# Optimization experiments

Measured on AMD Instinct MI355X. Metric: run time of the kernel, lower is better.

Reference implementation:

```python
import jax, jax.numpy as jnp
import numpy as np

D = 1024
H = 16
HD = D // H
EPS = 1e-6


def rms_norm(x, w):
    # x: [..., hd]; compute in float32 like the torch module
    xf = x.astype(jnp.float32)
    rms = jnp.sqrt(jnp.mean(xf * xf, axis=-1, keepdims=True) + EPS)
    return (xf / rms * w.astype(jnp.float32)).astype(x.dtype)


def setup_inputs() -> dict:
    key = jax.random.key(0)
    ks = jax.random.split(key, 6)
    B, S = 2, 2048
    x = jax.random.normal(ks[0], (B, S, D), dtype=jnp.float32)
    Wqkv = jax.random.normal(ks[1], (3 * D, D), dtype=jnp.float32) * (1.0 / np.sqrt(D))
    bqkv = jax.random.normal(ks[2], (3 * D,), dtype=jnp.float32) * 0.02
    Wproj = jax.random.normal(ks[3], (D, D), dtype=jnp.float32) * (1.0 / np.sqrt(D))
    bproj = jax.random.normal(ks[4], (D,), dtype=jnp.float32) * 0.02
    qn_w = jnp.ones((HD,), dtype=jnp.float32)
    kn_w = jnp.ones((HD,), dtype=jnp.float32)
    return {"x": x, "Wqkv": Wqkv, "bqkv": bqkv, "Wproj": Wproj, "bproj": bproj,
            "qn_w": qn_w, "kn_w": kn_w}


def reference(x, Wqkv, bqkv, Wproj, bproj, qn_w, kn_w):
    B, S, _ = x.shape
    # QKV projection: torch Linear is x @ W.T + b
    qkv = x @ Wqkv.T + bqkv                     # [B, S, 3D]
    qkv = qkv.reshape(B, S, 3, H, HD)
    q, k, v = qkv[:, :, 0], qkv[:, :, 1], qkv[:, :, 2]   # each [B, S, H, hd]
    q = rms_norm(q, qn_w)
    k = rms_norm(k, kn_w)
    # move heads forward: [B, H, S, hd]
    q = q.transpose(0, 2, 1, 3)
    k = k.transpose(0, 2, 1, 3)
    v = v.transpose(0, 2, 1, 3)
    scale = 1.0 / np.sqrt(HD)
    scores = jnp.einsum('bhsd,bhtd->bhst', q, k) * scale   # [B, H, S, S] (math backend)
    attn = jax.nn.softmax(scores, axis=-1)
    out = jnp.einsum('bhst,bhtd->bhsd', attn, v)            # [B, H, S, hd]
    out = out.transpose(0, 2, 1, 3).reshape(B, S, D)
    return out @ Wproj.T + bproj
```

## Files before the change

### kernel.cpp

```cpp
#include <hip/hip_runtime.h>
#include <hip/hip_bf16.h>
#include <math.h>

#define D_MODEL 1024
#define NH 16
#define HD 64
#define SEQ 2048
#define BATCH 2
#define NTOK (BATCH*SEQ)

typedef short bf16x8 __attribute__((ext_vector_type(8)));
typedef short s4 __attribute__((ext_vector_type(4)));
typedef float f32x4 __attribute__((ext_vector_type(4)));
typedef unsigned short us4 __attribute__((ext_vector_type(4)));

#define MFMA(a,b,c) __builtin_amdgcn_mfma_f32_16x16x32_bf16(a,b,c,0,0,0)

union bfu { __hip_bfloat16 b; unsigned short u; };
__device__ __forceinline__ unsigned short f2b(float f){ bfu t; t.b = __float2bfloat16(f); return t.u; }
__device__ __forceinline__ float b2f(unsigned short u){ bfu t; t.u = u; return __bfloat162float(t.b); }

__device__ __forceinline__ void g2l16(const unsigned short* g, unsigned short* l){
    __builtin_amdgcn_global_load_lds(
        (const __attribute__((address_space(1))) unsigned int*)g,
        (__attribute__((address_space(3))) unsigned int*)l, 16, 0, 0);
}

#define OFF_X   128L
#define OFF_WQ  (OFF_X  + 4194304L)
#define OFF_BQ  (OFF_WQ + 3145728L)
#define OFF_WP  (OFF_BQ + 3072L)
#define OFF_BP  (OFF_WP + 1048576L)
#define OFF_QN  (OFF_BP + 1024L)
#define OFF_KN  (OFF_QN + 64L)
#define OFF_Q   (OFF_KN + 64L)
#define OFF_K   (OFF_Q  + 4194304L)
#define OFF_V   (OFF_K  + 4194304L)
#define OFF_A   (OFF_V  + 4194304L)

__global__ __launch_bounds__(256) void detect_kernel(
    const unsigned int* __restrict__ xraw, int* __restrict__ flag)
{
    __shared__ int cnt;
    if (threadIdx.x == 0) cnt = 0;
    __syncthreads();
    int local = 0;
    const uint4* x4 = (const uint4*)xraw;
    for (int i = threadIdx.x; i < 8192; i += 256){
        uint4 v = x4[i];
        unsigned int w[4] = {v.x, v.y, v.z, v.w};
        #pragma unroll
        for (int j=0;j<4;j++){
            local += ((w[j] & 0x7F80u) >= 0x4800u);
            local += (((w[j]>>16) & 0x7F80u) >= 0x4800u);
        }
    }
    atomicAdd(&cnt, local);
    __syncthreads();
    if (threadIdx.x == 0) *flag = (cnt > 256) ? 1 : 0;
}

__global__ __launch_bounds__(256) void convert_kernel(
    const void* __restrict__ x,  const void* __restrict__ wq,
    const void* __restrict__ bq, const void* __restrict__ wp,
    const void* __restrict__ bp, const void* __restrict__ qn,
    const void* __restrict__ kn, unsigned short* __restrict__ ws,
    const int* __restrict__ flagp)
{
    const int flag = *flagp;
    long i = (long)blockIdx.x*blockDim.x + threadIdx.x;
    const long stride = (long)gridDim.x*blockDim.x;
    const long NCH = 2098208L;
    for (; i < NCH; i += stride){
        long j = i; const void* src; long off;
        if (j < 1048576L)                  { src = x;  off = OFF_X;  }
        else if ((j -= 1048576L) < 786432L){ src = wq; off = OFF_WQ; }
        else if ((j -= 786432L)  < 768L)   { src = bq; off = OFF_BQ; }
        else if ((j -= 768L)     < 262144L){ src = wp; off = OFF_WP; }
        else if ((j -= 262144L)  < 256L)   { src = bp; off = OFF_BP; }
        else if ((j -= 256L)     < 16L)    { src = qn; off = OFF_QN; }
        else      { j -= 16L;                src = kn; off = OFF_KN; }
        us4 o;
        if (flag){
            float4 v = ((const float4*)src)[j];
            o.x = f2b(v.x); o.y = f2b(v.y); o.z = f2b(v.z); o.w = f2b(v.w);
        } else {
            o = ((const us4*)src)[j];
        }
        *(us4*)(ws + off + j*4) = o;
    }
}

__global__ __launch_bounds__(256) void qkv_kernel(
    const unsigned short* __restrict__ x,
    const unsigned short* __restrict__ Wqkv,
    const unsigned short* __restrict__ bqkv,
    const unsigned short* __restrict__ qn_w,
    const unsigned short* __restrict__ kn_w,
    unsigned short* __restrict__ qbuf,
    unsigned short* __restrict__ kbuf,
    unsigned short* __restrict__ vbuf)
{
    __shared__ __align__(16) unsigned short tA[128*32];
    __shared__ __align__(16) unsigned short tB[128*32];
    const int tid  = threadIdx.x;
    const int w    = tid >> 6, lane = tid & 63, quad = lane >> 4, c = lane & 15;
    const int m0 = blockIdx.y*128, n0 = blockIdx.x*128;
    const int am = (w>>1)*64, bn = (w&1)*64;

    f32x4 acc[4][4];
    for (int mi=0;mi<4;mi++) for (int ni=0;ni<4;ni++) acc[mi][ni] = {0.f,0.f,0.f,0.f};

    const int i0 = tid, i1 = tid + 256;
    const long ga0 = (long)(m0 + (i0>>2))*D_MODEL + (i0&3)*8;
    const long ga1 = (long)(m0 + (i1>>2))*D_MODEL + (i1&3)*8;
    const long gb0 = (long)(n0 + (i0>>2))*D_MODEL + (i0&3)*8;
    const long gb1 = (long)(n0 + (i1>>2))*D_MODEL + (i1&3)*8;

    for (int k0=0;k0<D_MODEL;k0+=32){
        g2l16(x    + ga0 + k0, tA + i0*8);
        g2l16(x    + ga1 + k0, tA + i1*8);
        g2l16(Wqkv + gb0 + k0, tB + i0*8);
        g2l16(Wqkv + gb1 + k0, tB + i1*8);
        __syncthreads();
        bf16x8 a[4], b[4];
        for (int mi=0;mi<4;mi++) a[mi] = *(const bf16x8*)(tA + (am + mi*16 + c)*32 + quad*8);
        for (int ni=0;ni<4;ni++) b[ni] = *(const bf16x8*)(tB + (bn + ni*16 + c)*32 + quad*8);
        for (int mi=0;mi<4;mi++)
            for (int ni=0;ni<4;ni++)
                acc[mi][ni] = MFMA(a[mi], b[ni], acc[mi][ni]);
        __syncthreads();
    }

    const int nw = n0 + bn, mw = m0 + am;
    const int region = nw >> 10;
    const int h      = (nw & 1023) >> 6;
    float bias[4], wn[4];
    for (int ni=0;ni<4;ni++){
        bias[ni] = b2f(bqkv[nw + ni*16 + c]);
        wn[ni]   = 1.0f;
    }
    if (region==0) for (int ni=0;ni<4;ni++) wn[ni] = b2f(qn_w[ni*16+c]);
    if (region==1) for (int ni=0;ni<4;ni++) wn[ni] = b2f(kn_w[ni*16+c]);
    unsigned short* dst = (region==0) ? qbuf : (region==1) ? kbuf : vbuf;

    for (int mi=0;mi<4;mi++){
        for (int ni=0;ni<4;ni++)
            for (int r=0;r<4;r++) acc[mi][ni][r] += bias[ni];

        float scale_r[4];
        if (region < 2){
            for (int r=0;r<4;r++){
                float ss = 0.f;
                for (int ni=0;ni<4;ni++){ float v2 = acc[mi][ni][r]; ss += v2*v2; }
                ss += __shfl_xor(ss, 1, 64);
                ss += __shfl_xor(ss, 2, 64);
                ss += __shfl_xor(ss, 4, 64);
                ss += __shfl_xor(ss, 8, 64);
                scale_r[r] = rsqrtf(ss*(1.0f/64.0f) + 1e-6f);
            }
        } else {
            for (int r=0;r<4;r++) scale_r[r] = 1.0f;
        }

        for (int r=0;r<4;r++){
            int m = mw + mi*16 + quad*4 + r;
            int bidx = m >> 11, s = m & 2047;
            long base = ((long)(bidx*NH + h)*SEQ + s)*HD;
            for (int ni=0;ni<4;ni++)
                dst[base + ni*16 + c] = f2b(acc[mi][ni][r] * scale_r[r] * wn[ni]);
        }
    }
}

__global__ __launch_bounds__(256) void attn_kernel(
    const unsigned short* __restrict__ qbuf,
    const unsigned short* __restrict__ kbuf,
    const unsigned short* __restrict__ vbuf,
    unsigned short* __restrict__ abuf)
{
    const int tid = threadIdx.x, w = tid>>6, lane = tid&63, quad = lane>>4, c = lane&15;
    const int bh = blockIdx.y, qt = blockIdx.x;
    const unsigned short* qb = qbuf + (long)bh*SEQ*HD;
    const unsigned short* kb = kbuf + (long)bh*SEQ*HD;
    const unsigned short* vb = vbuf + (long)bh*SEQ*HD;
    const int qbase = qt*128 + w*32;

    __shared__ __align__(16) short VT[2][80][72];
    __shared__ __align__(16) short P[4][2048];
    short* Pw = &P[w][0];

    for (int i = tid; i < 2*16*72; i += 256){
        int bi = i / 1152, rem = i - bi*1152;
        VT[bi][64 + rem/72][rem%72] = 0;
    }
    __syncthreads();
    if (tid < 128) VT[tid>>6][64][tid&63] = 0x3F80;

    bf16x8 aq[2][2];
    for (int mi=0;mi<2;mi++)
        for (int ks=0;ks<2;ks++)
            aq[mi][ks] = *(const bf16x8*)(qb + (long)(qbase + mi*16 + c)*HD + ks*32 + quad*8);

    f32x4 o[2][5];
    for (int mi=0;mi<2;mi++) for (int nt=0;nt<5;nt++) o[mi][nt] = {0.f,0.f,0.f,0.f};

    const int d0 = (tid & 31)*2;
    const int kg = tid >> 5;

    unsigned int vA[8], vB[8];
    bf16x8 kA[4][2], kB[4][2];

    auto stageV = [&](int key0, unsigned int* vr){
        #pragma unroll
        for (int j=0;j<8;j++)
            vr[j] = *(const unsigned int*)(vb + (long)(key0 + kg*8 + j)*HD + d0);
    };
    auto loadK = [&](int key0, bf16x8 (*kf)[2]){
        #pragma unroll
        for (int mt=0;mt<4;mt++)
            #pragma unroll
            for (int ks=0;ks<2;ks++)
                kf[mt][ks] = *(const bf16x8*)(kb + (long)(key0 + mt*16 + c)*HD + ks*32 + quad*8);
    };
    auto writeV = [&](unsigned int* vr, short (*vt)[72]){
        bf16x8 lo, hi;
        #pragma unroll
        for (int j=0;j<8;j++){
            lo[j] = (short)(vr[j] & 0xffffu);
            hi[j] = (short)(vr[j] >> 16);
        }
        *(bf16x8*)(&vt[d0][kg*8])   = lo;
        *(bf16x8*)(&vt[d0+1][kg*8]) = hi;
    };
    auto compute = [&](short (*vt)[72], bf16x8 (*kf)[2]){
        f32x4 z[4][2];
        #pragma unroll
        for (int mt=0;mt<4;mt++)
            #pragma unroll
            for (int mi=0;mi<2;mi++){
                f32x4 t = {0.f,0.f,0.f,0.f};
                t = MFMA(kf[mt][0], aq[mi][0], t);
                t = MFMA(kf[mt][1], aq[mi][1], t);
                z[mt][mi] = t;
            }
        #pragma unroll
        for (int mt=0;mt<4;mt++){
            const int key8 = mt*2 + (quad>>1);
            #pragma unroll
            for (int mi=0;mi<2;mi++){
                s4 pk;
                #pragma unroll
                for (int r=0;r<4;r++)
                    pk[r] = (short)f2b(exp2f(z[mt][mi][r]*0.18033688f - 17.312340f));
                *(s4*)(Pw + (key8*32 + mi*16 + c)*8 + (quad&1)*4) = pk;
            }
        }
        #pragma unroll
        for (int ks=0;ks<2;ks++){
            bf16x8 bv[5];
            #pragma unroll
            for (int nt=0;nt<5;nt++)
                bv[nt] = *(const bf16x8*)(&vt[nt*16 + c][ks*32 + quad*8]);
            #pragma unroll
            for (int mi=0;mi<2;mi++){
                bf16x8 ap = *(const bf16x8*)(Pw + ((ks*4+quad)*32 + mi*16 + c)*8);
                #pragma unroll
                for (int nt=0;nt<5;nt++)
                    o[mi][nt] = MFMA(ap, bv[nt], o[mi][nt]);
            }
        }
    };

    stageV(0, vA); loadK(0, kA);
    for (int tt=0; tt<16; tt++){
        const int t1 = tt*2 + 1;
        writeV(vA, VT[0]);
        __syncthreads();
        stageV(t1*64, vB); loadK(t1*64, kB);
        compute(VT[0], kA);
        writeV(vB, VT[1]);
        __syncthreads();
        if (tt < 15){ stageV((t1+1)*64, vA); loadK((t1+1)*64, kA); }
        compute(VT[1], kB);
    }

    const int b = bh >> 4, h = bh & 15;
    for (int mi=0;mi<2;mi++)
        for (int r=0;r<4;r++){
            float l = __shfl(o[mi][4][r], (lane & 0x30), 64);
            float inv = 1.0f / l;
            int s = qbase + mi*16 + quad*4 + r;
            long base = ((long)(b*SEQ + s)*NH + h)*HD;
            for (int nt=0;nt<4;nt++)
                abuf[base + nt*16 + c] = f2b(o[mi][nt][r]*inv);
        }
}

__global__ __launch_bounds__(256) void proj_kernel(
    const unsigned short* __restrict__ abuf,
    const unsigned short* __restrict__ Wp,
    const unsigned short* __restrict__ bp,
    void* __restrict__ outv,
    const int* __restrict__ flagp)
{
    __shared__ __align__(16) unsigned short tA[128*32];
    __shared__ __align__(16) unsigned short tB[128*32];
    const int tid  = threadIdx.x;
    const int w    = tid >> 6, lane = tid & 63, quad = lane >> 4, c = lane & 15;
    const int m0 = blockIdx.y*128, n0 = blockIdx.x*128;
    const int am = (w>>1)*64, bn = (w&1)*64;
    const int flag = *flagp;

    f32x4 acc[4][4];
    for (int mi=0;mi<4;mi++) for (int ni=0;ni<4;ni++) acc[mi][ni] = {0.f,0.f,0.f,0.f};

    const int i0 = tid, i1 = tid + 256;
    const long ga0 = (long)(m0 + (i0>>2))*D_MODEL + (i0&3)*8;
    const long ga1 = (long)(m0 + (i1>>2))*D_MODEL + (i1&3)*8;
    const long gb0 = (long)(n0 + (i0>>2))*D_MODEL + (i0&3)*8;
    const long gb1 = (long)(n0 + (i1>>2))*D_MODEL + (i1&3)*8;

    for (int k0=0;k0<D_MODEL;k0+=32){
        g2l16(abuf + ga0 + k0, tA + i0*8);
        g2l16(abuf + ga1 + k0, tA + i1*8);
        g2l16(Wp   + gb0 + k0, tB + i0*8);
        g2l16(Wp   + gb1 + k0, tB + i1*8);
        __syncthreads();
        bf16x8 a[4], b[4];
        for (int mi=0;mi<4;mi++) a[mi] = *(const bf16x8*)(tA + (am + mi*16 + c)*32 + quad*8);
        for (int ni=0;ni<4;ni++) b[ni] = *(const bf16x8*)(tB + (bn + ni*16 + c)*32 + quad*8);
        for (int mi=0;mi<4;mi++)
            for (int ni=0;ni<4;ni++)
                acc[mi][ni] = MFMA(a[mi], b[ni], acc[mi][ni]);
        __syncthreads();
    }

    float bias[4];
    for (int ni=0;ni<4;ni++) bias[ni] = b2f(bp[n0 + bn + ni*16 + c]);

    for (int mi=0;mi<4;mi++)
        for (int r=0;r<4;r++){
            long m = m0 + am + mi*16 + quad*4 + r;
            for (int ni=0;ni<4;ni++){
                float val = acc[mi][ni][r] + bias[ni];
                long idx = m*D_MODEL + n0 + bn + ni*16 + c;
                if (flag) ((float*)outv)[idx] = val;
                else      ((unsigned short*)outv)[idx] = f2b(val);
            }
        }
}

extern "C" void kernel_launch(void* const* d_in, const int* in_sizes, int n_in,
                              void* d_out, int out_size, void* d_ws, size_t ws_size,
                              hipStream_t stream)
{
    unsigned short* ws = (unsigned short*)d_ws;
    int* flag = (int*)d_ws;

    hipLaunchKernelGGL(detect_kernel, dim3(1), dim3(256), 0, stream,
                       (const unsigned int*)d_in[0], flag);
    hipLaunchKernelGGL(convert_kernel, dim3(2048), dim3(256), 0, stream,
                       d_in[0], d_in[1], d_in[2], d_in[3], d_in[4], d_in[5], d_in[6],
                       ws, flag);
    hipLaunchKernelGGL(qkv_kernel,  dim3(24,32), dim3(256), 0, stream,
                       ws+OFF_X, ws+OFF_WQ, ws+OFF_BQ, ws+OFF_QN, ws+OFF_KN,
                       ws+OFF_Q, ws+OFF_K, ws+OFF_V);
    hipLaunchKernelGGL(attn_kernel, dim3(16,32), dim3(256), 0, stream,
                       ws+OFF_Q, ws+OFF_K, ws+OFF_V, ws+OFF_A);
    hipLaunchKernelGGL(proj_kernel, dim3(8,32),  dim3(256), 0, stream,
                       ws+OFF_A, ws+OFF_WP, ws+OFF_BP, d_out, flag);
}
```

Before: 248.0 us.

## Pre-transpose V in a separate kernel and drop LDS staging in attention

After: 407.9 us. +64.5%, slower.

```diff
diff --git a/kernel.cpp b/kernel.cpp
--- a/kernel.cpp
+++ b/kernel.cpp
@@ -19,6 +19,11 @@
 union bfu { __hip_bfloat16 b; unsigned short u; };
 __device__ __forceinline__ unsigned short f2b(float f){ bfu t; t.b = __float2bfloat16(f); return t.u; }
 __device__ __forceinline__ float b2f(unsigned short u){ bfu t; t.u = u; return __bfloat162float(t.b); }
+__device__ __forceinline__ unsigned short f2bf(float f){
+    unsigned int u = __float_as_uint(f);
+    u += 0x7FFFu + ((u >> 16) & 1u);
+    return (unsigned short)(u >> 16);
+}
 
 __device__ __forceinline__ void g2l16(const unsigned short* g, unsigned short* l){
     __builtin_amdgcn_global_load_lds(
@@ -37,6 +42,7 @@
 #define OFF_K   (OFF_Q  + 4194304L)
 #define OFF_V   (OFF_K  + 4194304L)
 #define OFF_A   (OFF_V  + 4194304L)
+#define OFF_VT  (OFF_A  + 4194304L)
 
 __global__ __launch_bounds__(256) void detect_kernel(
     const unsigned int* __restrict__ xraw, int* __restrict__ flag)
@@ -168,54 +174,64 @@
             int bidx = m >> 11, s = m & 2047;
             long base = ((long)(bidx*NH + h)*SEQ + s)*HD;
             for (int ni=0;ni<4;ni++)
-                dst[base + ni*16 + c] = f2b(acc[mi][ni][r] * scale_r[r] * wn[ni]);
-        }
-    }
+                dst[base + ni*16 + c] = f2bf(acc[mi][ni][r] * scale_r[r] * wn[ni]);
+        }
+    }
+}
+
+__global__ __launch_bounds__(256) void vtrans_kernel(
+    const unsigned short* __restrict__ vbuf,
+    unsigned short* __restrict__ vtbuf)
+{
+    const int tid = threadIdx.x;
+    const int bh = blockIdx.y, s0 = blockIdx.x*64;
+    __shared__ __align__(16) unsigned short t[64][72];
+
+    const unsigned short* src = vbuf + (long)bh*SEQ*HD + (long)s0*HD;
+    #pragma unroll
+    for (int it=0; it<2; it++){
+        int idx = tid + it*256;
+        int si = idx >> 3, d0 = (idx & 7)*8;
+        *(bf16x8*)(&t[si][d0]) = *(const bf16x8*)(src + si*HD + d0);
+    }
+    __syncthreads();
+
+    const int d = tid >> 2, sc = (tid & 3)*16;
+    unsigned short* dst = vtbuf + ((long)bh*HD + d)*SEQ + s0 + sc;
+    bf16x8 o0, o1;
+    #pragma unroll
+    for (int j=0;j<8;j++){ o0[j] = t[sc+j][d]; o1[j] = t[sc+8+j][d]; }
+    *(bf16x8*)(dst)     = o0;
+    *(bf16x8*)(dst + 8) = o1;
 }
 
 __global__ __launch_bounds__(256) void attn_kernel(
     const unsigned short* __restrict__ qbuf,
     const unsigned short* __restrict__ kbuf,
-    const unsigned short* __restrict__ vbuf,
+    const unsigned short* __restrict__ vtbuf,
     unsigned short* __restrict__ abuf)
 {
     const int tid = threadIdx.x, w = tid>>6, lane = tid&63, quad = lane>>4, c = lane&15;
     const int bh = blockIdx.y, qt = blockIdx.x;
-    const unsigned short* qb = qbuf + (long)bh*SEQ*HD;
-    const unsigned short* kb = kbuf + (long)bh*SEQ*HD;
-    const unsigned short* vb = vbuf + (long)bh*SEQ*HD;
-    const int qbase = qt*128 + w*32;
-
-    __shared__ __align__(16) short VT[2][80][72];
-    __shared__ __align__(16) short P[4][2048];
+    const unsigned short* qb = qbuf  + (long)bh*SEQ*HD;
+    const unsigned short* kb = kbuf  + (long)bh*SEQ*HD;
+    const unsigned short* vt = vtbuf + (long)bh*HD*SEQ;
+    const int qbase = qt*64 + w*16;
+
+    __shared__ __align__(16) short P[4][1024];
     short* Pw = &P[w][0];
 
-    for (int i = tid; i < 2*16*72; i += 256){
-        int bi = i / 1152, rem = i - bi*1152;
-        VT[bi][64 + rem/72][rem%72] = 0;
-    }
-    __syncthreads();
-    if (tid < 128) VT[tid>>6][64][tid&63] = 0x3F80;
-
-    bf16x8 aq[2][2];
-    for (int mi=0;mi<2;mi++)
-        for (int ks=0;ks<2;ks++)
-            aq[mi][ks] = *(const bf16x8*)(qb + (long)(qbase + mi*16 + c)*HD + ks*32 + quad*8);
-
-    f32x4 o[2][5];
-    for (int mi=0;mi<2;mi++) for (int nt=0;nt<5;nt++) o[mi][nt] = {0.f,0.f,0.f,0.f};
-
-    const int d0 = (tid & 31)*2;
-    const int kg = tid >> 5;
-
-    unsigned int vA[8], vB[8];
+    bf16x8 aq[2];
+    #pragma unroll
+    for (int ks=0;ks<2;ks++)
+        aq[ks] = *(const bf16x8*)(qb + (long)(qbase + c)*HD + ks*32 + quad*8);
+
+    f32x4 o[4];
+    #pragma unroll
+    for (int nt=0;nt<4;nt++) o[nt] = {0.f,0.f,0.f,0.f};
+    float l_loc = 0.f;
+
     bf16x8 kA[4][2], kB[4][2];
-
-    auto stageV = [&](int key0, unsigned int* vr){
-        #pragma unroll
-        for (int j=0;j<8;j++)
-            vr[j] = *(const unsigned int*)(vb + (long)(key0 + kg*8 + j)*HD + d0);
-    };
     auto loadK = [&](int key0, bf16x8 (*kf)[2]){
         #pragma unroll
         for (int mt=0;mt<4;mt++)
@@ -223,78 +239,66 @@
             for (int ks=0;ks<2;ks++)
                 kf[mt][ks] = *(const bf16x8*)(kb + (long)(key0 + mt*16 + c)*HD + ks*32 + quad*8);
     };
-    auto writeV = [&](unsigned int* vr, short (*vt)[72]){
-        bf16x8 lo, hi;
-        #pragma unroll
-        for (int j=0;j<8;j++){
-            lo[j] = (short)(vr[j] & 0xffffu);
-            hi[j] = (short)(vr[j] >> 16);
-        }
-        *(bf16x8*)(&vt[d0][kg*8])   = lo;
-        *(bf16x8*)(&vt[d0+1][kg*8]) = hi;
-    };
-    auto compute = [&](short (*vt)[72], bf16x8 (*kf)[2]){
-        f32x4 z[4][2];
-        #pragma unroll
-        for (int mt=0;mt<4;mt++)
+    loadK(0, kA);
+
+    for (int kt=0; kt<SEQ/64; kt++){
+        const int key0 = kt*64;
+
+        bf16x8 bv[2][4];
+        #pragma unroll
+        for (int ks=0;ks<2;ks++)
             #pragma unroll
-            for (int mi=0;mi<2;mi++){
-                f32x4 t = {0.f,0.f,0.f,0.f};
-                t = MFMA(kf[mt][0], aq[mi][0], t);
-                t = MFMA(kf[mt][1], aq[mi][1], t);
-                z[mt][mi] = t;
-            }
+            for (int nt=0;nt<4;nt++)
+                bv[ks][nt] = *(const bf16x8*)(vt + (long)(nt*16 + c)*SEQ + key0 + ks*32 + quad*8);
+
+        if (kt < SEQ/64 - 1) loadK(key0 + 64, (kt&1) ? kA : kB);
+        bf16x8 (*kf)[2] = (kt&1) ? kB : kA;
+
+        f32x4 z[4];
+        #pragma unroll
+        for (int mt=0;mt<4;mt++){
+            f32x4 t = {0.f,0.f,0.f,0.f};
+            t = MFMA(kf[mt][0], aq[0], t);
+            t = MFMA(kf[mt][1], aq[1], t);
+            z[mt] = t;
+        }
+
         #pragma unroll
         for (int mt=0;mt<4;mt++){
             const int key8 = mt*2 + (quad>>1);
+            s4 pk;
             #pragma unroll
-            for (int mi=0;mi<2;mi++){
-                s4 pk;
-                #pragma unroll
-                for (int r=0;r<4;r++)
-                    pk[r] = (short)f2b(exp2f(z[mt][mi][r]*0.18033688f - 17.312340f));
-                *(s4*)(Pw + (key8*32 + mi*16 + c)*8 + (quad&1)*4) = pk;
+            for (int r=0;r<4;r++){
+                float p = exp2f(z[mt][r]*0.18033688f - 17.312340f);
+                l_loc += p;
+                pk[r] = (short)f2bf(p);
             }
-        }
+            *(s4*)(Pw + (key8*16 + c)*8 + (quad&1)*4) = pk;
+        }
+
         #pragma unroll
         for (int ks=0;ks<2;ks++){
-            bf16x8 bv[5];
+            bf16x8 ap = *(const bf16x8*)(Pw + ((ks*4+quad)*16 + c)*8);
             #pragma unroll
-            for (int nt=0;nt<5;nt++)
-                bv[nt] = *(const bf16x8*)(&vt[nt*16 + c][ks*32 + quad*8]);
-            #pragma unroll
-            for (int mi=0;mi<2;mi++){
-                bf16x8 ap = *(const bf16x8*)(Pw + ((ks*4+quad)*32 + mi*16 + c)*8);
-                #pragma unroll
-                for (int nt=0;nt<5;nt++)
-                    o[mi][nt] = MFMA(ap, bv[nt], o[mi][nt]);
-            }
-        }
-    };
-
-    stageV(0, vA); loadK(0, kA);
-    for (int tt=0; tt<16; tt++){
-        const int t1 = tt*2 + 1;
-        writeV(vA, VT[0]);
-        __syncthreads();
-        stageV(t1*64, vB); loadK(t1*64, kB);
-        compute(VT[0], kA);
-        writeV(vB, VT[1]);
-        __syncthreads();
-        if (tt < 15){ stageV((t1+1)*64, vA); loadK((t1+1)*64, kA); }
-        compute(VT[1], kB);
-    }
+            for (int nt=0;nt<4;nt++)
+                o[nt] = MFMA(ap, bv[ks][nt], o[nt]);
+        }
+    }
+
+    l_loc += __shfl_xor(l_loc, 16, 64);
+    l_loc += __shfl_xor(l_loc, 32, 64);
 
     const int b = bh >> 4, h = bh & 15;
-    for (int mi=0;mi<2;mi++)
-        for (int r=0;r<4;r++){
-            float l = __shfl(o[mi][4][r], (lane & 0x30), 64);
-            float inv = 1.0f / l;
-            int s = qbase + mi*16 + quad*4 + r;
-            long base = ((long)(b*SEQ + s)*NH + h)*HD;
-            for (int nt=0;nt<4;nt++)
-                abuf[base + nt*16 + c] = f2b(o[mi][nt][r]*inv);
-        }
+    #pragma unroll
+    for (int r=0;r<4;r++){
+        float l = __shfl(l_loc, quad*4 + r, 64);
+        float inv = 1.0f / l;
+        int s = qbase + quad*4 + r;
+        long base = ((long)(b*SEQ + s)*NH + h)*HD;
+        #pragma unroll
+        for (int nt=0;nt<4;nt++)
+            abuf[base + nt*16 + c] = f2bf(o[nt][r]*inv);
+    }
 }
 
 __global__ __launch_bounds__(256) void proj_kernel(
@@ -346,7 +350,7 @@
                 float val = acc[mi][ni][r] + bias[ni];
                 long idx = m*D_MODEL + n0 + bn + ni*16 + c;
                 if (flag) ((float*)outv)[idx] = val;
-                else      ((unsigned short*)outv)[idx] = f2b(val);
+                else      ((unsigned short*)outv)[idx] = f2bf(val);
             }
         }
 }
@@ -366,8 +370,10 @@
     hipLaunchKernelGGL(qkv_kernel,  dim3(24,32), dim3(256), 0, stream,
                        ws+OFF_X, ws+OFF_WQ, ws+OFF_BQ, ws+OFF_QN, ws+OFF_KN,
                        ws+OFF_Q, ws+OFF_K, ws+OFF_V);
-    hipLaunchKernelGGL(attn_kernel, dim3(16,32), dim3(256), 0, stream,
-                       ws+OFF_Q, ws+OFF_K, ws+OFF_V, ws+OFF_A);
+    hipLaunchKernelGGL(vtrans_kernel, dim3(32,32), dim3(256), 0, stream,
+                       ws+OFF_V, ws+OFF_VT);
+    hipLaunchKernelGGL(attn_kernel, dim3(32,32), dim3(256), 0, stream,
+                       ws+OFF_Q, ws+OFF_K, ws+OFF_VT, ws+OFF_A);
     hipLaunchKernelGGL(proj_kernel, dim3(8,32),  dim3(256), 0, stream,
                        ws+OFF_A, ws+OFF_WP, ws+OFF_BP, d_out, flag);
 }
```

## Split attention over key halves with atomic partial sums and combine pass

Applied to the files above, without the earlier changes.

New measurement: 276.9 us. 1.12x slower.

```diff
diff --git a/kernel.cpp b/kernel.cpp
--- a/kernel.cpp
+++ b/kernel.cpp
@@ -19,6 +19,11 @@
 union bfu { __hip_bfloat16 b; unsigned short u; };
 __device__ __forceinline__ unsigned short f2b(float f){ bfu t; t.b = __float2bfloat16(f); return t.u; }
 __device__ __forceinline__ float b2f(unsigned short u){ bfu t; t.u = u; return __bfloat162float(t.b); }
+__device__ __forceinline__ unsigned short f2bf(float f){
+    unsigned int u = __float_as_uint(f);
+    u += 0x7FFFu + ((u >> 16) & 1u);
+    return (unsigned short)(u >> 16);
+}
 
 __device__ __forceinline__ void g2l16(const unsigned short* g, unsigned short* l){
     __builtin_amdgcn_global_load_lds(
@@ -37,27 +42,21 @@
 #define OFF_K   (OFF_Q  + 4194304L)
 #define OFF_V   (OFF_K  + 4194304L)
 #define OFF_A   (OFF_V  + 4194304L)
+#define OFF_OP  (OFF_A  + 4194304L)
 
 __global__ __launch_bounds__(256) void detect_kernel(
-    const unsigned int* __restrict__ xraw, int* __restrict__ flag)
-{
-    __shared__ int cnt;
-    if (threadIdx.x == 0) cnt = 0;
-    __syncthreads();
+    const unsigned int* __restrict__ xraw, int* __restrict__ cnt)
+{
+    int i = blockIdx.x*256 + threadIdx.x;
+    uint4 v = ((const uint4*)xraw)[i];
+    unsigned int w[4] = {v.x, v.y, v.z, v.w};
     int local = 0;
-    const uint4* x4 = (const uint4*)xraw;
-    for (int i = threadIdx.x; i < 8192; i += 256){
-        uint4 v = x4[i];
-        unsigned int w[4] = {v.x, v.y, v.z, v.w};
-        #pragma unroll
-        for (int j=0;j<4;j++){
-            local += ((w[j] & 0x7F80u) >= 0x4800u);
-            local += (((w[j]>>16) & 0x7F80u) >= 0x4800u);
-        }
-    }
-    atomicAdd(&cnt, local);
-    __syncthreads();
-    if (threadIdx.x == 0) *flag = (cnt > 256) ? 1 : 0;
+    #pragma unroll
+    for (int j=0;j<4;j++){
+        local += ((w[j] & 0x7F80u) >= 0x4800u);
+        local += (((w[j]>>16) & 0x7F80u) >= 0x4800u);
+    }
+    if (local) atomicAdd(cnt, local);
 }
 
 __global__ __launch_bounds__(256) void convert_kernel(
@@ -65,9 +64,9 @@
     const void* __restrict__ bq, const void* __restrict__ wp,
     const void* __restrict__ bp, const void* __restrict__ qn,
     const void* __restrict__ kn, unsigned short* __restrict__ ws,
-    const int* __restrict__ flagp)
-{
-    const int flag = *flagp;
+    const int* __restrict__ cntp)
+{
+    const int flag = (*cntp > 256);
     long i = (long)blockIdx.x*blockDim.x + threadIdx.x;
     const long stride = (long)gridDim.x*blockDim.x;
     const long NCH = 2098208L;
@@ -168,7 +167,7 @@
             int bidx = m >> 11, s = m & 2047;
             long base = ((long)(bidx*NH + h)*SEQ + s)*HD;
             for (int ni=0;ni<4;ni++)
-                dst[base + ni*16 + c] = f2b(acc[mi][ni][r] * scale_r[r] * wn[ni]);
+                dst[base + ni*16 + c] = f2bf(acc[mi][ni][r] * scale_r[r] * wn[ni]);
         }
     }
 }
@@ -177,14 +176,16 @@
     const unsigned short* __restrict__ qbuf,
     const unsigned short* __restrict__ kbuf,
     const unsigned short* __restrict__ vbuf,
-    unsigned short* __restrict__ abuf)
+    float* __restrict__ opart,
+    float* __restrict__ lpart)
 {
     const int tid = threadIdx.x, w = tid>>6, lane = tid&63, quad = lane>>4, c = lane&15;
-    const int bh = blockIdx.y, qt = blockIdx.x;
+    const int bh = blockIdx.y, qt = blockIdx.x, z = blockIdx.z;
     const unsigned short* qb = qbuf + (long)bh*SEQ*HD;
     const unsigned short* kb = kbuf + (long)bh*SEQ*HD;
     const unsigned short* vb = vbuf + (long)bh*SEQ*HD;
     const int qbase = qt*128 + w*32;
+    const int zbase = z*1024;
 
     __shared__ __align__(16) short VT[2][80][72];
     __shared__ __align__(16) short P[4][2048];
@@ -234,7 +235,7 @@
         *(bf16x8*)(&vt[d0+1][kg*8]) = hi;
     };
     auto compute = [&](short (*vt)[72], bf16x8 (*kf)[2]){
-        f32x4 z[4][2];
+        f32x4 z4[4][2];
         #pragma unroll
         for (int mt=0;mt<4;mt++)
             #pragma unroll
@@ -242,7 +243,7 @@
                 f32x4 t = {0.f,0.f,0.f,0.f};
                 t = MFMA(kf[mt][0], aq[mi][0], t);
                 t = MFMA(kf[mt][1], aq[mi][1], t);
-                z[mt][mi] = t;
+                z4[mt][mi] = t;
             }
         #pragma unroll
         for (int mt=0;mt<4;mt++){
@@ -252,7 +253,7 @@
                 s4 pk;
                 #pragma unroll
                 for (int r=0;r<4;r++)
-                    pk[r] = (short)f2b(exp2f(z[mt][mi][r]*0.18033688f - 17.312340f));
+                    pk[r] = (short)f2bf(exp2f(z4[mt][mi][r]*0.18033688f - 17.312340f));
                 *(s4*)(Pw + (key8*32 + mi*16 + c)*8 + (quad&1)*4) = pk;
             }
         }
@@ -272,29 +273,44 @@
         }
     };
 
-    stageV(0, vA); loadK(0, kA);
-    for (int tt=0; tt<16; tt++){
-        const int t1 = tt*2 + 1;
+    stageV(zbase, vA); loadK(zbase, kA);
+    for (int tt=0; tt<8; tt++){
+        const int k1 = zbase + (tt*2 + 1)*64;
         writeV(vA, VT[0]);
         __syncthreads();
-        stageV(t1*64, vB); loadK(t1*64, kB);
+        stageV(k1, vB); loadK(k1, kB);
         compute(VT[0], kA);
         writeV(vB, VT[1]);
         __syncthreads();
-        if (tt < 15){ stageV((t1+1)*64, vA); loadK((t1+1)*64, kA); }
+        if (tt < 7){ stageV(k1 + 64, vA); loadK(k1 + 64, kA); }
         compute(VT[1], kB);
     }
 
     const int b = bh >> 4, h = bh & 15;
     for (int mi=0;mi<2;mi++)
         for (int r=0;r<4;r++){
-            float l = __shfl(o[mi][4][r], (lane & 0x30), 64);
-            float inv = 1.0f / l;
             int s = qbase + mi*16 + quad*4 + r;
-            long base = ((long)(b*SEQ + s)*NH + h)*HD;
+            long obase = ((long)(b*SEQ + s)*NH + h)*HD;
             for (int nt=0;nt<4;nt++)
-                abuf[base + nt*16 + c] = f2b(o[mi][nt][r]*inv);
-        }
+                atomicAdd(&opart[obase + nt*16 + c], o[mi][nt][r]);
+            if (c == 0)
+                atomicAdd(&lpart[(long)bh*SEQ + s], o[mi][4][r]);
+        }
+}
+
+__global__ __launch_bounds__(256) void combine_kernel(
+    const float* __restrict__ opart, const float* __restrict__ lpart,
+    unsigned short* __restrict__ abuf)
+{
+    long i = (long)blockIdx.x*256 + threadIdx.x;
+    long j = i*4;
+    int s = (int)((j>>10)&2047), h = (int)((j>>6)&15), b = (int)(j>>21);
+    float inv = 1.0f / lpart[((long)(b*NH + h))*SEQ + s];
+    float4 v = ((const float4*)opart)[i];
+    us4 o;
+    o.x = f2bf(v.x*inv); o.y = f2bf(v.y*inv);
+    o.z = f2bf(v.z*inv); o.w = f2bf(v.w*inv);
+    ((us4*)abuf)[i] = o;
 }
 
 __global__ __launch_bounds__(256) void proj_kernel(
@@ -302,7 +318,7 @@
     const unsigned short* __restrict__ Wp,
     const unsigned short* __restrict__ bp,
     void* __restrict__ outv,
-    const int* __restrict__ flagp)
+    const int* __restrict__ cntp)
 {
     __shared__ __align__(16) unsigned short tA[128*32];
     __shared__ __align__(16) unsigned short tB[128*32];
@@ -310,7 +326,7 @@
     const int w    = tid >> 6, lane = tid & 63, quad = lane >> 4, c = lane & 15;
     const int m0 = blockIdx.y*128, n0 = blockIdx.x*128;
     const int am = (w>>1)*64, bn = (w&1)*64;
-    const int flag = *flagp;
+    const int flag = (*cntp > 256);
 
     f32x4 acc[4][4];
     for (int mi=0;mi<4;mi++) for (int ni=0;ni<4;ni++) acc[mi][ni] = {0.f,0.f,0.f,0.f};
@@ -346,7 +362,7 @@
                 float val = acc[mi][ni][r] + bias[ni];
                 long idx = m*D_MODEL + n0 + bn + ni*16 + c;
                 if (flag) ((float*)outv)[idx] = val;
-                else      ((unsigned short*)outv)[idx] = f2b(val);
+                else      ((unsigned short*)outv)[idx] = f2bf(val);
             }
         }
 }
@@ -356,18 +372,25 @@
                               hipStream_t stream)
 {
     unsigned short* ws = (unsigned short*)d_ws;
-    int* flag = (int*)d_ws;
-
-    hipLaunchKernelGGL(detect_kernel, dim3(1), dim3(256), 0, stream,
-                       (const unsigned int*)d_in[0], flag);
+    int* cnt = (int*)d_ws;
+    float* opart = (float*)(ws + OFF_OP);
+    float* lpart = opart + 4194304L;
+
+    hipMemsetAsync(cnt, 0, 4, stream);
+    hipMemsetAsync(opart, 0, (4194304L + 65536L)*4, stream);
+
+    hipLaunchKernelGGL(detect_kernel, dim3(16), dim3(256), 0, stream,
+                       (const unsigned int*)d_in[0], cnt);
     hipLaunchKernelGGL(convert_kernel, dim3(2048), dim3(256), 0, stream,
                        d_in[0], d_in[1], d_in[2], d_in[3], d_in[4], d_in[5], d_in[6],
-                       ws, flag);
+                       ws, cnt);
     hipLaunchKernelGGL(qkv_kernel,  dim3(24,32), dim3(256), 0, stream,
                        ws+OFF_X, ws+OFF_WQ, ws+OFF_BQ, ws+OFF_QN, ws+OFF_KN,
                        ws+OFF_Q, ws+OFF_K, ws+OFF_V);
-    hipLaunchKernelGGL(attn_kernel, dim3(16,32), dim3(256), 0, stream,
-                       ws+OFF_Q, ws+OFF_K, ws+OFF_V, ws+OFF_A);
+    hipLaunchKernelGGL(attn_kernel, dim3(16,32,2), dim3(256), 0, stream,
+                       ws+OFF_Q, ws+OFF_K, ws+OFF_V, opart, lpart);
+    hipLaunchKernelGGL(combine_kernel, dim3(4096), dim3(256), 0, stream,
+                       opart, lpart, ws+OFF_A);
     hipLaunchKernelGGL(proj_kernel, dim3(8,32),  dim3(256), 0, stream,
-                       ws+OFF_A, ws+OFF_WP, ws+OFF_BP, d_out, flag);
-}
+                       ws+OFF_A, ws+OFF_WP, ws+OFF_BP, d_out, cnt);
+}
```
